# Optimization experiments

Hardware: AMD Instinct MI355X
Metric: run time of the kernel (lower is better)

## Reference

```python
import jax, jax.numpy as jnp
import numpy as np

D_MODEL = 1024
N_HEADS = 16
D_FF = 4096
LN_EPS = 1e-5


def setup_inputs() -> dict:
    key = jax.random.key(0)
    ks = jax.random.split(key, 16)
    B, T, D, F = 2, 2048, D_MODEL, D_FF
    s = 1.0 / np.sqrt(D)
    inp = {
        'x': jax.random.normal(ks[0], (B, T, D), dtype=jnp.float32),
        'wq': jax.random.normal(ks[1], (D, D), dtype=jnp.float32) * s,
        'bq': jnp.zeros((D,), jnp.float32),
        'wk': jax.random.normal(ks[2], (D, D), dtype=jnp.float32) * s,
        'bk': jnp.zeros((D,), jnp.float32),
        'wv': jax.random.normal(ks[3], (D, D), dtype=jnp.float32) * s,
        'bv': jnp.zeros((D,), jnp.float32),
        'wo': jax.random.normal(ks[4], (D, D), dtype=jnp.float32) * s,
        'bo': jnp.zeros((D,), jnp.float32),
        'ln1_g': jnp.ones((D,), jnp.float32),
        'ln1_b': jnp.zeros((D,), jnp.float32),
        'w1': jax.random.normal(ks[5], (D, F), dtype=jnp.float32) * s,
        'b1': jnp.zeros((F,), jnp.float32),
        'w2': jax.random.normal(ks[6], (F, D), dtype=jnp.float32) * (1.0 / np.sqrt(F)),
        'b2': jnp.zeros((D,), jnp.float32),
        'ln2_g': jnp.ones((D,), jnp.float32),
        'ln2_b': jnp.zeros((D,), jnp.float32),
    }
    return inp


def _layernorm(x, g, b):
    mu = jnp.mean(x, axis=-1, keepdims=True)
    var = jnp.mean(jnp.square(x - mu), axis=-1, keepdims=True)
    return (x - mu) * jax.lax.rsqrt(var + LN_EPS) * g + b


def reference(x, wq, bq, wk, bk, wv, bv, wo, bo, ln1_g, ln1_b, w1, b1, w2, b2, ln2_g, ln2_b):
    B, T, D = x.shape
    H, dk = N_HEADS, D // N_HEADS
    # QKV projections -> [B, H, T, dk]
    def proj(w, b):
        return (x @ w + b).reshape(B, T, H, dk).transpose(0, 2, 1, 3)
    q, k, v = proj(wq, bq), proj(wk, bk), proj(wv, bv)
    scores = jnp.einsum('bhtd,bhsd->bhts', q, k) / np.sqrt(dk)
    causal = jnp.tril(jnp.ones((T, T), dtype=bool))
    scores = jnp.where(causal, scores, -jnp.inf)
    attn = jax.nn.softmax(scores, axis=-1)  # dropout p=0 (eval)
    out = jnp.einsum('bhts,bhsd->bhtd', attn, v)
    out = out.transpose(0, 2, 1, 3).reshape(B, T, D) @ wo + bo
    h = _layernorm(x + out, ln1_g, ln1_b)
    ff = jax.nn.relu(h @ w1 + b1) @ w2 + b2
    return _layernorm(h + ff, ln2_g, ln2_b)
```

## Files before the change

kernel.cpp:

```cpp
#include <hip/hip_runtime.h>
#include <math.h>

#define D_MODEL 1024
#define N_HEADSC 16
#define DKH 64
#define D_FFC 4096

typedef short bf16x8 __attribute__((ext_vector_type(8)));
typedef float f32x4 __attribute__((ext_vector_type(4)));

#define GLOAD_LDS16(g, l)                                                      \
    __builtin_amdgcn_global_load_lds(                                          \
        (const __attribute__((address_space(1))) void*)(g),                    \
        (__attribute__((address_space(3))) void*)(l), 16, 0, 0)

__device__ inline unsigned short f2bf(float f) {
    unsigned u = __float_as_uint(f);
    u += 0x7fff + ((u >> 16) & 1);
    return (unsigned short)(u >> 16);
}
__device__ inline float bf2f(unsigned short h) {
    return __uint_as_float(((unsigned)h) << 16);
}

template<int BN_, bool RELU, bool RES, bool SPLIT>
__launch_bounds__(256)
__global__ void gemm_sb(const unsigned short* __restrict__ A2,
                        const unsigned short* __restrict__ Bt2,
                        const float* __restrict__ bias,
                        const float* __restrict__ res,
                        void* __restrict__ Cout,
                        int K, int N) {
    constexpr int BM_ = 128;
    constexpr int WCOLS = BN_ / 2;
    constexpr int NT = WCOLS / 16;
    __shared__ unsigned short As[BM_ * 32];
    __shared__ unsigned short Bs[BN_ * 32];
    const int tid = threadIdx.x;
    const int l = tid & 63, w = tid >> 6;
    const int wrow = w >> 1, wcol = w & 1;
    const int brow = blockIdx.y * BM_;
    const int bcol = blockIdx.x * BN_;
    const size_t ldk = 2 * (size_t)K;

    f32x4 acc[4][NT];
    #pragma unroll
    for (int mt = 0; mt < 4; ++mt)
        #pragma unroll
        for (int nt = 0; nt < NT; ++nt) acc[mt][nt] = (f32x4){0.f, 0.f, 0.f, 0.f};

    const int r0 = tid >> 2;
    const int c0 = (tid & 3) * 8;
    const int lr = l & 15, kg = (l >> 4) * 8;

    #pragma unroll 1
    for (int t = 0; t < 3; ++t) {
        const int aBase = (t == 2) ? K : 0;
        const int wBase = (t == 1) ? K : 0;
        #pragma unroll 1
        for (int kb = 0; kb < K; kb += 32) {
            GLOAD_LDS16(A2 + (size_t)(brow + r0) * ldk + aBase + kb + c0, &As[tid * 8]);
            GLOAD_LDS16(A2 + (size_t)(brow + 64 + r0) * ldk + aBase + kb + c0, &As[(256 + tid) * 8]);
            GLOAD_LDS16(Bt2 + (size_t)(bcol + r0) * ldk + wBase + kb + c0, &Bs[tid * 8]);
            if constexpr (BN_ == 128) {
                GLOAD_LDS16(Bt2 + (size_t)(bcol + 64 + r0) * ldk + wBase + kb + c0, &Bs[(256 + tid) * 8]);
            }
            __syncthreads();

            bf16x8 af[4], bfr[NT];
            #pragma unroll
            for (int mt = 0; mt < 4; ++mt)
                af[mt] = *(const bf16x8*)&As[(wrow * 64 + mt * 16 + lr) * 32 + kg];
            #pragma unroll
            for (int nt = 0; nt < NT; ++nt)
                bfr[nt] = *(const bf16x8*)&Bs[(wcol * WCOLS + nt * 16 + lr) * 32 + kg];
            #pragma unroll
            for (int mt = 0; mt < 4; ++mt)
                #pragma unroll
                for (int nt = 0; nt < NT; ++nt)
                    acc[mt][nt] = __builtin_amdgcn_mfma_f32_16x16x32_bf16(
                        af[mt], bfr[nt], acc[mt][nt], 0, 0, 0);
            __syncthreads();
        }
    }

    const int lg = l >> 4;
    #pragma unroll
    for (int mt = 0; mt < 4; ++mt) {
        #pragma unroll
        for (int nt = 0; nt < NT; ++nt) {
            #pragma unroll
            for (int j = 0; j < 4; ++j) {
                const int row = brow + wrow * 64 + mt * 16 + lg * 4 + j;
                const int col = bcol + wcol * WCOLS + nt * 16 + lr;
                float v = acc[mt][nt][j] + bias[col];
                if (RES) v += res[(size_t)row * N + col];
                if (RELU) v = fmaxf(v, 0.f);
                if (SPLIT) {
                    unsigned short hi = f2bf(v);
                    unsigned short lo = f2bf(v - bf2f(hi));
                    unsigned short* C = (unsigned short*)Cout;
                    C[(size_t)row * (2 * (size_t)N) + col] = hi;
                    C[(size_t)row * (2 * (size_t)N) + N + col] = lo;
                } else {
                    ((float*)Cout)[(size_t)row * N + col] = v;
                }
            }
        }
    }
}

__launch_bounds__(256)
__global__ void gemm_qkv(const unsigned short* __restrict__ A2,
                         const unsigned short* __restrict__ Bt2,
                         const float* __restrict__ bias,
                         unsigned short* __restrict__ qk2,
                         unsigned short* __restrict__ vT2,
                         int K, int N) {
    __shared__ unsigned short As[128 * 32];
    __shared__ unsigned short Bs[128 * 32];
    const int tid = threadIdx.x;
    const int l = tid & 63, w = tid >> 6;
    const int wrow = w >> 1, wcol = w & 1;
    const int brow = blockIdx.y * 128;
    const int bcol = blockIdx.x * 128;
    const size_t ldk = 2 * (size_t)K;

    f32x4 acc[4][4];
    #pragma unroll
    for (int mt = 0; mt < 4; ++mt)
        #pragma unroll
        for (int nt = 0; nt < 4; ++nt) acc[mt][nt] = (f32x4){0.f, 0.f, 0.f, 0.f};

    const int r0 = tid >> 2;
    const int c0 = (tid & 3) * 8;
    const int lr = l & 15, kg = (l >> 4) * 8;

    #pragma unroll 1
    for (int t = 0; t < 3; ++t) {
        const int aBase = (t == 2) ? K : 0;
        const int wBase = (t == 1) ? K : 0;
        #pragma unroll 1
        for (int kb = 0; kb < K; kb += 32) {
            GLOAD_LDS16(A2 + (size_t)(brow + r0) * ldk + aBase + kb + c0, &As[tid * 8]);
            GLOAD_LDS16(A2 + (size_t)(brow + 64 + r0) * ldk + aBase + kb + c0, &As[(256 + tid) * 8]);
            GLOAD_LDS16(Bt2 + (size_t)(bcol + r0) * ldk + wBase + kb + c0, &Bs[tid * 8]);
            GLOAD_LDS16(Bt2 + (size_t)(bcol + 64 + r0) * ldk + wBase + kb + c0, &Bs[(256 + tid) * 8]);
            __syncthreads();

            bf16x8 af[4], bfr[4];
            #pragma unroll
            for (int mt = 0; mt < 4; ++mt)
                af[mt] = *(const bf16x8*)&As[(wrow * 64 + mt * 16 + lr) * 32 + kg];
            #pragma unroll
            for (int nt = 0; nt < 4; ++nt)
                bfr[nt] = *(const bf16x8*)&Bs[(wcol * 64 + nt * 16 + lr) * 32 + kg];
            #pragma unroll
            for (int mt = 0; mt < 4; ++mt)
                #pragma unroll
                for (int nt = 0; nt < 4; ++nt)
                    acc[mt][nt] = __builtin_amdgcn_mfma_f32_16x16x32_bf16(
                        af[mt], bfr[nt], acc[mt][nt], 0, 0, 0);
            __syncthreads();
        }
    }

    const int lg = l >> 4;
    #pragma unroll
    for (int mt = 0; mt < 4; ++mt) {
        #pragma unroll
        for (int nt = 0; nt < 4; ++nt) {
            #pragma unroll
            for (int j = 0; j < 4; ++j) {
                const int row = brow + wrow * 64 + mt * 16 + lg * 4 + j;
                const int col = bcol + wcol * 64 + nt * 16 + lr;
                float v = acc[mt][nt][j] + bias[col];
                if (col < 1024) v *= 0.125f;
                const unsigned short hi = f2bf(v);
                const unsigned short lo = f2bf(v - bf2f(hi));
                if (col < 2048) {
                    qk2[(size_t)row * 4096 + col] = hi;
                    qk2[(size_t)row * 4096 + 2048 + col] = lo;
                } else {
                    const int vc = col - 2048, hh = vc >> 6, dd = vc & 63;
                    const int bb = row >> 11, tt = row & 2047;
                    const size_t basev = ((size_t)((bb * 16 + hh) * 2) * 64 + dd) * 2048 + tt;
                    vT2[basev] = hi;
                    vT2[basev + (size_t)64 * 2048] = lo;
                }
            }
        }
    }
}

__launch_bounds__(256)
__global__ void attn_mfma(const unsigned short* __restrict__ qk2,
                          const unsigned short* __restrict__ vT2,
                          unsigned short* __restrict__ ao2) {
    constexpr int T = 2048;
    __shared__ unsigned short KsHi[4096], KsLo[4096], VsHi[4096], VsLo[4096];

    const int tid = threadIdx.x;
    const int l = tid & 63, w = tid >> 6;
    const int g = l >> 4, q15 = l & 15;
    const int bh = blockIdx.x, b = bh >> 4, h = bh & 15;
    const int qbr = blockIdx.y;
    const int qb = (qbr < 8) ? qbr : 23 - qbr;
    const int qw = qb * 128 + w * 32;

    bf16x8 qhi[2][2], qlo[2][2];
    #pragma unroll
    for (int qf = 0; qf < 2; ++qf)
        #pragma unroll
        for (int kc = 0; kc < 2; ++kc) {
            const size_t m = (size_t)b * T + qw + qf * 16 + q15;
            qhi[qf][kc] = *(const bf16x8*)&qk2[m * 4096 + h * 64 + kc * 32 + g * 8];
            qlo[qf][kc] = *(const bf16x8*)&qk2[m * 4096 + 2048 + h * 64 + kc * 32 + g * 8];
        }

    f32x4 out[2][4];
    #pragma unroll
    for (int qf = 0; qf < 2; ++qf)
        #pragma unroll
        for (int df = 0; df < 4; ++df) out[qf][df] = (f32x4){0.f, 0.f, 0.f, 0.f};
    float mreg[2] = {-1e30f, -1e30f};
    float lreg[2] = {0.f, 0.f};

    const int ntiles = 2 * qb + 2;
    const size_t kvVbase0 = ((size_t)(bh * 2 + 0) * 64) * 2048;
    const size_t kvVbase1 = ((size_t)(bh * 2 + 1) * 64) * 2048;

    for (int kt = 0; kt < ntiles; ++kt) {
        const int kv0 = kt * 64;
        #pragma unroll
        for (int rr = 0; rr < 2; ++rr) {
            const int slot = rr * 256 + tid;
            const int row = slot >> 3, c = slot & 7;
            const int cs = (c ^ (row & 7)) * 8;
            const size_t krow = (size_t)(b * T + kv0 + row) * 4096;
            GLOAD_LDS16(qk2 + krow + 1024 + h * 64 + cs, &KsHi[slot * 8]);
            GLOAD_LDS16(qk2 + krow + 3072 + h * 64 + cs, &KsLo[slot * 8]);
            GLOAD_LDS16(vT2 + kvVbase0 + (size_t)row * 2048 + kv0 + cs, &VsHi[slot * 8]);
            GLOAD_LDS16(vT2 + kvVbase1 + (size_t)row * 2048 + kv0 + cs, &VsLo[slot * 8]);
        }
        __syncthreads();

        if (kv0 <= qw + 31) {
            f32x4 sT[4][2];
            #pragma unroll
            for (int kvf = 0; kvf < 4; ++kvf)
                #pragma unroll
                for (int qf = 0; qf < 2; ++qf) sT[kvf][qf] = (f32x4){0.f, 0.f, 0.f, 0.f};
            #pragma unroll
            for (int kvf = 0; kvf < 4; ++kvf) {
                const int rowk = kvf * 16 + q15, sw = rowk & 7;
                bf16x8 khi[2], klo[2];
                #pragma unroll
                for (int kc = 0; kc < 2; ++kc) {
                    khi[kc] = *(const bf16x8*)&KsHi[rowk * 64 + ((kc * 4 + g) ^ sw) * 8];
                    klo[kc] = *(const bf16x8*)&KsLo[rowk * 64 + ((kc * 4 + g) ^ sw) * 8];
                }
                #pragma unroll
                for (int qf = 0; qf < 2; ++qf)
                    #pragma unroll
                    for (int kc = 0; kc < 2; ++kc) {
                        sT[kvf][qf] = __builtin_amdgcn_mfma_f32_16x16x32_bf16(khi[kc], qhi[qf][kc], sT[kvf][qf], 0, 0, 0);
                        sT[kvf][qf] = __builtin_amdgcn_mfma_f32_16x16x32_bf16(khi[kc], qlo[qf][kc], sT[kvf][qf], 0, 0, 0);
                        sT[kvf][qf] = __builtin_amdgcn_mfma_f32_16x16x32_bf16(klo[kc], qhi[qf][kc], sT[kvf][qf], 0, 0, 0);
                    }
            }
            if (kv0 + 63 > qw) {
                #pragma unroll
                for (int kvf = 0; kvf < 4; ++kvf)
                    #pragma unroll
                    for (int qf = 0; qf < 2; ++qf)
                        #pragma unroll
                        for (int j = 0; j < 4; ++j) {
                            const int kvg = kv0 + kvf * 16 + g * 4 + j;
                            const int qg = qw + qf * 16 + q15;
                            if (kvg > qg) sT[kvf][qf][j] = -1e30f;
                        }
            }
            float alphaq[2];
            #pragma unroll
            for (int qf = 0; qf < 2; ++qf) {
                float tmax = -1e30f;
                #pragma unroll
                for (int kvf = 0; kvf < 4; ++kvf)
                    #pragma unroll
                    for (int j = 0; j < 4; ++j) tmax = fmaxf(tmax, sT[kvf][qf][j]);
                tmax = fmaxf(tmax, __shfl_xor(tmax, 16));
                tmax = fmaxf(tmax, __shfl_xor(tmax, 32));
                const float mn = fmaxf(mreg[qf], tmax);
                alphaq[qf] = __expf(mreg[qf] - mn);
                mreg[qf] = mn;
                float ts = 0.f;
                #pragma unroll
                for (int kvf = 0; kvf < 4; ++kvf)
                    #pragma unroll
                    for (int j = 0; j < 4; ++j) {
                        const float p = __expf(sT[kvf][qf][j] - mn);
                        sT[kvf][qf][j] = p;
                        ts += p;
                    }
                ts += __shfl_xor(ts, 16);
                ts += __shfl_xor(ts, 32);
                lreg[qf] = lreg[qf] * alphaq[qf] + ts;
            }
            #pragma unroll
            for (int qf = 0; qf < 2; ++qf) {
                float av[4];
                #pragma unroll
                for (int j = 0; j < 4; ++j) av[j] = __shfl(alphaq[qf], g * 4 + j);
                #pragma unroll
                for (int df = 0; df < 4; ++df)
                    #pragma unroll
                    for (int j = 0; j < 4; ++j) out[qf][df][j] *= av[j];
            }
            #pragma unroll
            for (int kc = 0; kc < 2; ++kc) {
                bf16x8 phi[2], plo[2];
                #pragma unroll
                for (int qf = 0; qf < 2; ++qf) {
                    #pragma unroll
                    for (int m = 0; m < 8; ++m) {
                        const int src = ((g & 1) * 2 + (m >> 2)) * 16 + q15;
                        const float t0 = __shfl(sT[kc * 2 + 0][qf][m & 3], src);
                        const float t1 = __shfl(sT[kc * 2 + 1][qf][m & 3], src);
                        const float pvv = (g >= 2) ? t1 : t0;
                        const unsigned short hi = f2bf(pvv);
                        phi[qf][m] = (short)hi;
                        plo[qf][m] = (short)f2bf(pvv - bf2f(hi));
                    }
                }
                #pragma unroll
                for (int df = 0; df < 4; ++df) {
                    const int rowv = df * 16 + q15, swv = rowv & 7;
                    const bf16x8 vhi = *(const bf16x8*)&VsHi[rowv * 64 + ((kc * 4 + g) ^ swv) * 8];
                    const bf16x8 vlo = *(const bf16x8*)&VsLo[rowv * 64 + ((kc * 4 + g) ^ swv) * 8];
                    #pragma unroll
                    for (int qf = 0; qf < 2; ++qf) {
                        out[qf][df] = __builtin_amdgcn_mfma_f32_16x16x32_bf16(phi[qf], vhi, out[qf][df], 0, 0, 0);
                        out[qf][df] = __builtin_amdgcn_mfma_f32_16x16x32_bf16(phi[qf], vlo, out[qf][df], 0, 0, 0);
                        out[qf][df] = __builtin_amdgcn_mfma_f32_16x16x32_bf16(plo[qf], vhi, out[qf][df], 0, 0, 0);
                    }
                }
            }
        }
        __syncthreads();
    }

    #pragma unroll
    for (int qf = 0; qf < 2; ++qf) {
        const float linv = 1.f / lreg[qf];
        float lv[4];
        #pragma unroll
        for (int j = 0; j < 4; ++j) lv[j] = __shfl(linv, g * 4 + j);
        #pragma unroll
        for (int df = 0; df < 4; ++df)
            #pragma unroll
            for (int j = 0; j < 4; ++j) {
                const float v = out[qf][df][j] * lv[j];
                const unsigned short hi = f2bf(v);
                const unsigned short lo = f2bf(v - bf2f(hi));
                const size_t m = (size_t)b * T + qw + qf * 16 + g * 4 + j;
                const int col = h * 64 + df * 16 + q15;
                ao2[m * 2048 + col] = hi;
                ao2[m * 2048 + 1024 + col] = lo;
            }
    }
}

__launch_bounds__(256)
__global__ void wsplit_t_k(const float* __restrict__ W, unsigned short* __restrict__ Wt2,
                           int K, int N, int ldo) {
    __shared__ float Tt[32][33];
    const int tx = threadIdx.x & 31, ty = threadIdx.x >> 5;
    const int k0 = blockIdx.y * 32, n0 = blockIdx.x * 32;
    #pragma unroll
    for (int i = 0; i < 4; ++i)
        Tt[i * 8 + ty][tx] = W[(size_t)(k0 + i * 8 + ty) * N + n0 + tx];
    __syncthreads();
    #pragma unroll
    for (int i = 0; i < 4; ++i) {
        const int r = i * 8 + ty;
        const float v = Tt[tx][r];
        const unsigned short hi = f2bf(v);
        const unsigned short lo = f2bf(v - bf2f(hi));
        Wt2[(size_t)(n0 + r) * ldo + k0 + tx] = hi;
        Wt2[(size_t)(n0 + r) * ldo + K + k0 + tx] = lo;
    }
}

__launch_bounds__(256)
__global__ void split2_k(const float* __restrict__ X, unsigned short* __restrict__ X2) {
    const int idx = (blockIdx.x * 256 + threadIdx.x) * 4;
    const int r = idx >> 10, c = idx & 1023;
    float4 v = *(const float4*)&X[idx];
    ushort4 h, lo;
    h.x = f2bf(v.x); lo.x = f2bf(v.x - bf2f(h.x));
    h.y = f2bf(v.y); lo.y = f2bf(v.y - bf2f(h.y));
    h.z = f2bf(v.z); lo.z = f2bf(v.z - bf2f(h.z));
    h.w = f2bf(v.w); lo.w = f2bf(v.w - bf2f(h.w));
    *(ushort4*)&X2[(size_t)r * 2048 + c] = h;
    *(ushort4*)&X2[(size_t)r * 2048 + 1024 + c] = lo;
}

__global__ void biascat_k(const float* a, const float* b, const float* c, float* o) {
    const int i = blockIdx.x * 256 + threadIdx.x;
    o[i] = (i < 1024) ? a[i] : ((i < 2048) ? b[i - 1024] : c[i - 2048]);
}

template<bool SPLIT>
__launch_bounds__(256)
__global__ void ln_k(const float* __restrict__ X, const float* __restrict__ g,
                     const float* __restrict__ b, float* __restrict__ Y,
                     unsigned short* __restrict__ Y2) {
    const int row = blockIdx.x;
    const int tid = threadIdx.x;
    const size_t off = (size_t)row * D_MODEL + tid * 4;
    float4 v = *(const float4*)&X[off];
    float s = v.x + v.y + v.z + v.w;
    float s2 = v.x * v.x + v.y * v.y + v.z * v.z + v.w * v.w;
    #pragma unroll
    for (int o = 1; o < 64; o <<= 1) { s += __shfl_xor(s, o); s2 += __shfl_xor(s2, o); }
    __shared__ float red[8];
    const int wid = tid >> 6, lane = tid & 63;
    if (lane == 0) { red[wid] = s; red[4 + wid] = s2; }
    __syncthreads();
    s = red[0] + red[1] + red[2] + red[3];
    s2 = red[4] + red[5] + red[6] + red[7];
    const float mu = s * (1.f / D_MODEL);
    const float var = s2 * (1.f / D_MODEL) - mu * mu;
    const float rst = rsqrtf(var + 1e-5f);
    float4 gv = *(const float4*)&g[tid * 4];
    float4 bv = *(const float4*)&b[tid * 4];
    float4 ov;
    ov.x = (v.x - mu) * rst * gv.x + bv.x;
    ov.y = (v.y - mu) * rst * gv.y + bv.y;
    ov.z = (v.z - mu) * rst * gv.z + bv.z;
    ov.w = (v.w - mu) * rst * gv.w + bv.w;
    *(float4*)&Y[off] = ov;
    if (SPLIT) {
        ushort4 h4, lo4;
        h4.x = f2bf(ov.x); lo4.x = f2bf(ov.x - bf2f(h4.x));
        h4.y = f2bf(ov.y); lo4.y = f2bf(ov.y - bf2f(h4.y));
        h4.z = f2bf(ov.z); lo4.z = f2bf(ov.z - bf2f(h4.z));
        h4.w = f2bf(ov.w); lo4.w = f2bf(ov.w - bf2f(h4.w));
        *(ushort4*)&Y2[(size_t)row * 2048 + tid * 4] = h4;
        *(ushort4*)&Y2[(size_t)row * 2048 + 1024 + tid * 4] = lo4;
    }
}

extern "C" void kernel_launch(void* const* d_in, const int* in_sizes, int n_in,
                              void* d_out, int out_size, void* d_ws, size_t ws_size,
                              hipStream_t stream) {
    (void)in_sizes; (void)n_in; (void)out_size; (void)ws_size;
    const float* x    = (const float*)d_in[0];
    const float* wq   = (const float*)d_in[1];
    const float* bq   = (const float*)d_in[2];
    const float* wk   = (const float*)d_in[3];
    const float* bk   = (const float*)d_in[4];
    const float* wv   = (const float*)d_in[5];
    const float* bv   = (const float*)d_in[6];
    const float* wo   = (const float*)d_in[7];
    const float* bo   = (const float*)d_in[8];
    const float* ln1g = (const float*)d_in[9];
    const float* ln1b = (const float*)d_in[10];
    const float* w1   = (const float*)d_in[11];
    const float* b1   = (const float*)d_in[12];
    const float* w2   = (const float*)d_in[13];
    const float* b2   = (const float*)d_in[14];
    const float* ln2g = (const float*)d_in[15];
    const float* ln2b = (const float*)d_in[16];
    float* out = (float*)d_out;

    const int B = 2, T = 2048, D = D_MODEL, F = D_FFC;
    const int M = B * T;

    char* ws = (char*)d_ws;
    const size_t MB = 1048576;
    unsigned short* qk2    = (unsigned short*)(ws + 0);
    unsigned short* mid2   = (unsigned short*)(ws + 0);
    unsigned short* vT2    = (unsigned short*)(ws + 32 * MB);
    unsigned short* x2     = (unsigned short*)(ws + 48 * MB);
    unsigned short* ao2    = (unsigned short*)(ws + 48 * MB);
    unsigned short* h12    = (unsigned short*)(ws + 64 * MB);
    unsigned short* wslotA = (unsigned short*)(ws + 80 * MB);
    unsigned short* wslotB = (unsigned short*)(ws + 96 * MB);
    float*          bqkv   = (float*)(ws + 112 * MB);

    dim3 blk(256);

    wsplit_t_k<<<dim3(32, 32), blk, 0, stream>>>(wq, wslotA + 0    * (size_t)2048, D, D, 2048);
    wsplit_t_k<<<dim3(32, 32), blk, 0, stream>>>(wk, wslotA + 1024 * (size_t)2048, D, D, 2048);
    wsplit_t_k<<<dim3(32, 32), blk, 0, stream>>>(wv, wslotA + 2048 * (size_t)2048, D, D, 2048);
    wsplit_t_k<<<dim3(32, 32), blk, 0, stream>>>(wo, wslotB, D, D, 2048);
    split2_k<<<4096, blk, 0, stream>>>(x, x2);
    biascat_k<<<12, blk, 0, stream>>>(bq, bk, bv, bqkv);

    gemm_qkv<<<dim3(24, 32), blk, 0, stream>>>(x2, wslotA, bqkv, qk2, vT2, D, 3 * D);

    wsplit_t_k<<<dim3(128, 32), blk, 0, stream>>>(w1, wslotA, D, F, 2048);

    attn_mfma<<<dim3(32, 16), blk, 0, stream>>>(qk2, vT2, ao2);

    gemm_sb<64, false, true, false><<<dim3(16, 32), blk, 0, stream>>>(
        ao2, wslotB, bo, x, out, D, D);

    wsplit_t_k<<<dim3(32, 128), blk, 0, stream>>>(w2, wslotB, F, D, 8192);

    ln_k<true><<<M, blk, 0, stream>>>(out, ln1g, ln1b, out, h12);

    gemm_sb<128, true, false, true><<<dim3(32, 32), blk, 0, stream>>>(
        h12, wslotA, b1, nullptr, mid2, D, F);

    gemm_sb<64, false, true, false><<<dim3(16, 32), blk, 0, stream>>>(
        mid2, wslotB, b2, out, out, F, D);

    ln_k<false><<<M, blk, 0, stream>>>(out, ln2g, ln2b, out, nullptr);
}
```

Baseline: 790.4 us.

## Fuse split-bf16 passes into one K loop and add XCD block swizzle

The GEMM kernels previously ran three separate K sweeps (hi*hi, hi*lo, lo*hi), reloading A and B tiles from global memory each time. Now one K loop stages both the hi and lo halves of each tile in separate LDS buffers and issues all three MFMAs per fragment pair. This removes two-thirds of the barrier-separated iterations and gives each load more MFMA work. It also adds an XCD-aware block remap so neighbouring tiles run on the same XCD for L2 reuse. The cost is twice the LDS per block and more live fragment registers, which may lower occupancy.

```diff
diff --git a/kernel.cpp b/kernel.cpp
--- a/kernel.cpp
+++ b/kernel.cpp
@@ -21,6 +21,15 @@
 }
 __device__ inline float bf2f(unsigned short h) {
     return __uint_as_float(((unsigned)h) << 16);
+}
+
+__device__ inline void xcd_swz(int& bx, int& by) {
+    const int nwg = gridDim.x * gridDim.y;
+    int lin = blockIdx.y * gridDim.x + blockIdx.x;
+    const int q = nwg >> 3;
+    lin = (lin & 7) * q + (lin >> 3);
+    bx = lin % gridDim.x;
+    by = lin / gridDim.x;
 }
 
 template<int BN_, bool RELU, bool RES, bool SPLIT>
@@ -34,13 +43,15 @@
     constexpr int BM_ = 128;
     constexpr int WCOLS = BN_ / 2;
     constexpr int NT = WCOLS / 16;
-    __shared__ unsigned short As[BM_ * 32];
-    __shared__ unsigned short Bs[BN_ * 32];
+    __shared__ unsigned short AsH[BM_ * 32], AsL[BM_ * 32];
+    __shared__ unsigned short BsH[BN_ * 32], BsL[BN_ * 32];
     const int tid = threadIdx.x;
     const int l = tid & 63, w = tid >> 6;
     const int wrow = w >> 1, wcol = w & 1;
-    const int brow = blockIdx.y * BM_;
-    const int bcol = blockIdx.x * BN_;
+    int bx, by;
+    xcd_swz(bx, by);
+    const int brow = by * BM_;
+    const int bcol = bx * BN_;
     const size_t ldk = 2 * (size_t)K;
 
     f32x4 acc[4][NT];
@@ -54,34 +65,45 @@
     const int lr = l & 15, kg = (l >> 4) * 8;
 
     #pragma unroll 1
-    for (int t = 0; t < 3; ++t) {
-        const int aBase = (t == 2) ? K : 0;
-        const int wBase = (t == 1) ? K : 0;
-        #pragma unroll 1
-        for (int kb = 0; kb < K; kb += 32) {
-            GLOAD_LDS16(A2 + (size_t)(brow + r0) * ldk + aBase + kb + c0, &As[tid * 8]);
-            GLOAD_LDS16(A2 + (size_t)(brow + 64 + r0) * ldk + aBase + kb + c0, &As[(256 + tid) * 8]);
-            GLOAD_LDS16(Bt2 + (size_t)(bcol + r0) * ldk + wBase + kb + c0, &Bs[tid * 8]);
-            if constexpr (BN_ == 128) {
-                GLOAD_LDS16(Bt2 + (size_t)(bcol + 64 + r0) * ldk + wBase + kb + c0, &Bs[(256 + tid) * 8]);
-            }
-            __syncthreads();
-
-            bf16x8 af[4], bfr[NT];
-            #pragma unroll
-            for (int mt = 0; mt < 4; ++mt)
-                af[mt] = *(const bf16x8*)&As[(wrow * 64 + mt * 16 + lr) * 32 + kg];
-            #pragma unroll
-            for (int nt = 0; nt < NT; ++nt)
-                bfr[nt] = *(const bf16x8*)&Bs[(wcol * WCOLS + nt * 16 + lr) * 32 + kg];
-            #pragma unroll
-            for (int mt = 0; mt < 4; ++mt)
-                #pragma unroll
-                for (int nt = 0; nt < NT; ++nt)
-                    acc[mt][nt] = __builtin_amdgcn_mfma_f32_16x16x32_bf16(
-                        af[mt], bfr[nt], acc[mt][nt], 0, 0, 0);
-            __syncthreads();
-        }
+    for (int kb = 0; kb < K; kb += 32) {
+        const size_t arow0 = (size_t)(brow + r0) * ldk;
+        const size_t arow1 = (size_t)(brow + 64 + r0) * ldk;
+        GLOAD_LDS16(A2 + arow0 + kb + c0, &AsH[tid * 8]);
+        GLOAD_LDS16(A2 + arow1 + kb + c0, &AsH[(256 + tid) * 8]);
+        GLOAD_LDS16(A2 + arow0 + K + kb + c0, &AsL[tid * 8]);
+        GLOAD_LDS16(A2 + arow1 + K + kb + c0, &AsL[(256 + tid) * 8]);
+        const size_t brow0 = (size_t)(bcol + r0) * ldk;
+        GLOAD_LDS16(Bt2 + brow0 + kb + c0, &BsH[tid * 8]);
+        GLOAD_LDS16(Bt2 + brow0 + K + kb + c0, &BsL[tid * 8]);
+        if constexpr (BN_ == 128) {
+            const size_t brow1 = (size_t)(bcol + 64 + r0) * ldk;
+            GLOAD_LDS16(Bt2 + brow1 + kb + c0, &BsH[(256 + tid) * 8]);
+            GLOAD_LDS16(Bt2 + brow1 + K + kb + c0, &BsL[(256 + tid) * 8]);
+        }
+        __syncthreads();
+
+        bf16x8 ah[4], al[4], bh[NT], bl[NT];
+        #pragma unroll
+        for (int mt = 0; mt < 4; ++mt) {
+            const int ar = (wrow * 64 + mt * 16 + lr) * 32 + kg;
+            ah[mt] = *(const bf16x8*)&AsH[ar];
+            al[mt] = *(const bf16x8*)&AsL[ar];
+        }
+        #pragma unroll
+        for (int nt = 0; nt < NT; ++nt) {
+            const int br = (wcol * WCOLS + nt * 16 + lr) * 32 + kg;
+            bh[nt] = *(const bf16x8*)&BsH[br];
+            bl[nt] = *(const bf16x8*)&BsL[br];
+        }
+        #pragma unroll
+        for (int mt = 0; mt < 4; ++mt)
+            #pragma unroll
+            for (int nt = 0; nt < NT; ++nt) {
+                acc[mt][nt] = __builtin_amdgcn_mfma_f32_16x16x32_bf16(ah[mt], bh[nt], acc[mt][nt], 0, 0, 0);
+                acc[mt][nt] = __builtin_amdgcn_mfma_f32_16x16x32_bf16(ah[mt], bl[nt], acc[mt][nt], 0, 0, 0);
+                acc[mt][nt] = __builtin_amdgcn_mfma_f32_16x16x32_bf16(al[mt], bh[nt], acc[mt][nt], 0, 0, 0);
+            }
+        __syncthreads();
     }
 
     const int lg = l >> 4;
@@ -117,13 +139,15 @@
                          unsigned short* __restrict__ qk2,
                          unsigned short* __restrict__ vT2,
                          int K, int N) {
-    __shared__ unsigned short As[128 * 32];
-    __shared__ unsigned short Bs[128 * 32];
+    __shared__ unsigned short AsH[128 * 32], AsL[128 * 32];
+    __shared__ unsigned short BsH[128 * 32], BsL[128 * 32];
     const int tid = threadIdx.x;
     const int l = tid & 63, w = tid >> 6;
     const int wrow = w >> 1, wcol = w & 1;
-    const int brow = blockIdx.y * 128;
-    const int bcol = blockIdx.x * 128;
+    int bx, by;
+    xcd_swz(bx, by);
+    const int brow = by * 128;
+    const int bcol = bx * 128;
     const size_t ldk = 2 * (size_t)K;
 
     f32x4 acc[4][4];
@@ -137,32 +161,43 @@
     const int lr = l & 15, kg = (l >> 4) * 8;
 
     #pragma unroll 1
-    for (int t = 0; t < 3; ++t) {
-        const int aBase = (t == 2) ? K : 0;
-        const int wBase = (t == 1) ? K : 0;
-        #pragma unroll 1
-        for (int kb = 0; kb < K; kb += 32) {
-            GLOAD_LDS16(A2 + (size_t)(brow + r0) * ldk + aBase + kb + c0, &As[tid * 8]);
-            GLOAD_LDS16(A2 + (size_t)(brow + 64 + r0) * ldk + aBase + kb + c0, &As[(256 + tid) * 8]);
-            GLOAD_LDS16(Bt2 + (size_t)(bcol + r0) * ldk + wBase + kb + c0, &Bs[tid * 8]);
-            GLOAD_LDS16(Bt2 + (size_t)(bcol + 64 + r0) * ldk + wBase + kb + c0, &Bs[(256 + tid) * 8]);
-            __syncthreads();
-
-            bf16x8 af[4], bfr[4];
-            #pragma unroll
-            for (int mt = 0; mt < 4; ++mt)
-                af[mt] = *(const bf16x8*)&As[(wrow * 64 + mt * 16 + lr) * 32 + kg];
-            #pragma unroll
-            for (int nt = 0; nt < 4; ++nt)
-                bfr[nt] = *(const bf16x8*)&Bs[(wcol * 64 + nt * 16 + lr) * 32 + kg];
-            #pragma unroll
-            for (int mt = 0; mt < 4; ++mt)
-                #pragma unroll
-                for (int nt = 0; nt < 4; ++nt)
-                    acc[mt][nt] = __builtin_amdgcn_mfma_f32_16x16x32_bf16(
-                        af[mt], bfr[nt], acc[mt][nt], 0, 0, 0);
-            __syncthreads();
-        }
+    for (int kb = 0; kb < K; kb += 32) {
+        const size_t arow0 = (size_t)(brow + r0) * ldk;
+        const size_t arow1 = (size_t)(brow + 64 + r0) * ldk;
+        GLOAD_LDS16(A2 + arow0 + kb + c0, &AsH[tid * 8]);
+        GLOAD_LDS16(A2 + arow1 + kb + c0, &AsH[(256 + tid) * 8]);
+        GLOAD_LDS16(A2 + arow0 + K + kb + c0, &AsL[tid * 8]);
+        GLOAD_LDS16(A2 + arow1 + K + kb + c0, &AsL[(256 + tid) * 8]);
+        const size_t brow0 = (size_t)(bcol + r0) * ldk;
+        const size_t brow1 = (size_t)(bcol + 64 + r0) * ldk;
+        GLOAD_LDS16(Bt2 + brow0 + kb + c0, &BsH[tid * 8]);
+        GLOAD_LDS16(Bt2 + brow1 + kb + c0, &BsH[(256 + tid) * 8]);
+        GLOAD_LDS16(Bt2 + brow0 + K + kb + c0, &BsL[tid * 8]);
+        GLOAD_LDS16(Bt2 + brow1 + K + kb + c0, &BsL[(256 + tid) * 8]);
+        __syncthreads();
+
+        bf16x8 ah[4], al[4], bh[4], bl[4];
+        #pragma unroll
+        for (int mt = 0; mt < 4; ++mt) {
+            const int ar = (wrow * 64 + mt * 16 + lr) * 32 + kg;
+            ah[mt] = *(const bf16x8*)&AsH[ar];
+            al[mt] = *(const bf16x8*)&AsL[ar];
+        }
+        #pragma unroll
+        for (int nt = 0; nt < 4; ++nt) {
+            const int br = (wcol * 64 + nt * 16 + lr) * 32 + kg;
+            bh[nt] = *(const bf16x8*)&BsH[br];
+            bl[nt] = *(const bf16x8*)&BsL[br];
+        }
+        #pragma unroll
+        for (int mt = 0; mt < 4; ++mt)
+            #pragma unroll
+            for (int nt = 0; nt < 4; ++nt) {
+                acc[mt][nt] = __builtin_amdgcn_mfma_f32_16x16x32_bf16(ah[mt], bh[nt], acc[mt][nt], 0, 0, 0);
+                acc[mt][nt] = __builtin_amdgcn_mfma_f32_16x16x32_bf16(ah[mt], bl[nt], acc[mt][nt], 0, 0, 0);
+                acc[mt][nt] = __builtin_amdgcn_mfma_f32_16x16x32_bf16(al[mt], bh[nt], acc[mt][nt], 0, 0, 0);
+            }
+        __syncthreads();
     }
 
     const int lg = l >> 4;
```

Result: faster. 673.3 us (-14.8%).
